# Performance work log

Hardware: AMD Instinct MI355X
Metric: run time of the kernel (lower is better)

Reference implementation:

```python
import jax, jax.numpy as jnp
import numpy as np

B, C, H, W = 8, 96, 160, 320
MH, MW = 4, 4

def setup_inputs() -> dict:
    key = jax.random.key(0)
    k1, k2 = jax.random.split(key)
    feat1 = jax.random.normal(k1, (B, C, H, W), dtype=jnp.float32)
    feat2 = jax.random.normal(k2, (B, C, H, W), dtype=jnp.float32)
    return {"feat1": feat1, "feat2": feat2, "max_offset_h": MH, "max_offset_w": MW}

def reference(feat1, feat2, max_offset_h, max_offset_w):
    # feat1, feat2: [B, C, H, W]
    # cost[b, d, h, w] = sum_c feat1[b,c,h,w] * feat2[b,c,h+dh,w+dw]
    # with (dh, dw) enumerating the (2*mh+1)*(2*mw+1) offset window and
    # zero padding outside image boundaries.
    b, c, h, w = feat1.shape
    mh, mw = max_offset_h, max_offset_w
    padded = jnp.pad(feat2, ((0, 0), (0, 0), (mh, mh), (mw, mw)))
    costs = []
    for dh in range(2 * mh + 1):
        for dw in range(2 * mw + 1):
            shifted = jax.lax.dynamic_slice(padded, (0, 0, dh, dw), (b, c, h, w))
            costs.append(jnp.sum(feat1 * shifted, axis=1))  # [B, H, W]
    return jnp.stack(costs, axis=1)  # [B, (2mh+1)*(2mw+1), H, W]
```

## Files before the change

### kernel.cpp

```cpp
#include <hip/hip_runtime.h>

#define B_   8
#define C_   96
#define H_   160
#define W_   320
#define ND   9
#define NDD  81
#define TH   16
#define TW   16
#define KC   6
#define NCH  16
#define F2ROWS 18
#define F2STRIDE 28
#define F2PLANE (F2ROWS*F2STRIDE)
#define BUFW (KC*F2PLANE)
#define NBUF 3
#define LDSWORDS (NBUF*BUFW)

#define AS1 __attribute__((address_space(1)))
#define AS3 __attribute__((address_space(3)))

__device__ __forceinline__ void gld16(const float* gp, float* lp) {
    __builtin_amdgcn_global_load_lds((const AS1 float*)gp,
                                     (AS3 float*)(unsigned long long)lp, 16, 0, 0);
}

__global__ __launch_bounds__(192, 2)
void corr_kernel(const float* __restrict__ f1g,
                 const float* __restrict__ f2g,
                 float* __restrict__ out)
{
    __shared__ float lds[LDSWORDS];

    const int tid  = threadIdx.x;
    const int wave = tid >> 6;
    const int lane = tid & 63;
    const int row  = lane >> 2;
    const int colb = (lane & 3) << 2;

    const int bid  = blockIdx.x;
    const int ebid = (bid & 7) * 600 + (bid >> 3);
    const int b    = ebid / 600;
    const int t6   = ebid - b * 600;
    const int g    = t6 % 3;
    const int tile = t6 / 3;
    const int by   = tile / 20, bx = tile - by * 20;
    const int x0 = bx * TW, y0 = by * TH;
    const int HWi  = H_ * W_;
    const int r0   = y0 + 3 * g - 4;

    const float* f1b = f1g + (size_t)b * C_ * HWi;
    const float* f2b = f2g + (size_t)b * C_ * HWi;

    const float* f1p = f1b + (y0 + row) * W_ + x0 + colb;

    int so0, so1; bool p0, p1;
    {
        int s, r, c, gy, gx;
        s = lane;      r = s / 7; c = (s - 7 * r) << 2;
        gy = r0 + r;   gx = x0 - 4 + c;
        p0 = (c < 24) & (gy >= 0) & (gy < H_) & (gx >= 0) & (gx <= W_ - 4);
        so0 = gy * W_ + gx;
        s = 64 + lane; r = s / 7; c = (s - 7 * r) << 2;
        gy = r0 + r;   gx = x0 - 4 + c;
        p1 = (s < 126) & (c < 24) & (gy >= 0) & (gy < H_) & (gx >= 0) & (gx <= W_ - 4);
        so1 = gy * W_ + gx;
    }

    const int o0 = (row + wave) * F2STRIDE + colb;

    auto stage = [&](int cb, int bufb) {
#pragma unroll
        for (int j = 0; j < 2; ++j) {
            const int ch = 3 * j + wave;
            const int co = (cb + ch) * HWi;
            float* l = &lds[bufb + ch * F2PLANE];
            if (p0) gld16(f2b + co + so0, l);
            if (p1) gld16(f2b + co + so1, l + 256);
        }
    };

    float4 acc0, acc1, acc2, acc3, acc4, acc5, acc6, acc7, acc8;
    acc0 = acc1 = acc2 = acc3 = acc4 = acc5 = acc6 = acc7 = acc8 = make_float4(0.f, 0.f, 0.f, 0.f);
    float4 P0, P1, P2, P3, P4, P5;

#define F1LOAD(cb) {                                         \
        P0 = *(const float4*)(f1p + (cb) * HWi);             \
        P1 = *(const float4*)(f1p + ((cb) + 1) * HWi);       \
        P2 = *(const float4*)(f1p + ((cb) + 2) * HWi);       \
        P3 = *(const float4*)(f1p + ((cb) + 3) * HWi);       \
        P4 = *(const float4*)(f1p + ((cb) + 4) * HWi);       \
        P5 = *(const float4*)(f1p + ((cb) + 5) * HWi); }

#define STEPD(A, P, e0, e1, e2, e3)                          \
        A.x = fmaf(P.x, e0, A.x);                            \
        A.y = fmaf(P.y, e1, A.y);                            \
        A.z = fmaf(P.z, e2, A.z);                            \
        A.w = fmaf(P.w, e3, A.w);

#define COMPC(c, RB, P) {                                                         \
        const float4 q0 = *(const float4*)&lds[(RB) + c * F2PLANE + o0];          \
        const float4 q1 = *(const float4*)&lds[(RB) + c * F2PLANE + o0 + 4];      \
        const float4 q2 = *(const float4*)&lds[(RB) + c * F2PLANE + o0 + 8];      \
        STEPD(acc0, P, q0.x, q0.y, q0.z, q0.w)                                    \
        STEPD(acc1, P, q0.y, q0.z, q0.w, q1.x)                                    \
        STEPD(acc2, P, q0.z, q0.w, q1.x, q1.y)                                    \
        STEPD(acc3, P, q0.w, q1.x, q1.y, q1.z)                                    \
        STEPD(acc4, P, q1.x, q1.y, q1.z, q1.w)                                    \
        STEPD(acc5, P, q1.y, q1.z, q1.w, q2.x)                                    \
        STEPD(acc6, P, q1.z, q1.w, q2.x, q2.y)                                    \
        STEPD(acc7, P, q1.w, q2.x, q2.y, q2.z)                                    \
        STEPD(acc8, P, q2.x, q2.y, q2.z, q2.w)                                    \
    }
#define CHUNK(RB) COMPC(0,RB,P0) COMPC(1,RB,P1) COMPC(2,RB,P2) \
                  COMPC(3,RB,P3) COMPC(4,RB,P4) COMPC(5,RB,P5)

    for (int t = tid; t < LDSWORDS; t += 192) lds[t] = 0.f;
    __syncthreads();

    stage(0, 0);
    stage(KC, BUFW);

#pragma unroll 1
    for (int k = 0; k < NCH; ++k) {
        if (k < NCH - 1) { asm volatile("s_waitcnt vmcnt(4)" ::: "memory"); }
        else             { asm volatile("s_waitcnt vmcnt(0)" ::: "memory"); }
        __builtin_amdgcn_s_barrier();
        __builtin_amdgcn_sched_barrier(0);
        F1LOAD(KC * k)
        __builtin_amdgcn_sched_barrier(0);
        if (k + 2 < NCH) stage(KC * (k + 2), ((k + 2) % NBUF) * BUFW);
        __builtin_amdgcn_sched_barrier(0);
        const int rb_ = (k % NBUF) * BUFW;
        CHUNK(rb_)
    }

    const int dh = 3 * g + wave;
    const int gy = y0 + row;
    const int gx = x0 + colb;
#define STORED(d) {                                                                 \
        float* op_ = out + (size_t)((b * NDD + dh * ND + d) * H_ + gy) * W_ + gx;   \
        *(float4*)op_ = acc##d; }
    STORED(0) STORED(1) STORED(2) STORED(3) STORED(4)
    STORED(5) STORED(6) STORED(7) STORED(8)
}

extern "C" void kernel_launch(void* const* d_in, const int* in_sizes, int n_in,
                              void* d_out, int out_size, void* d_ws, size_t ws_size,
                              hipStream_t stream)
{
    const float* f1 = (const float*)d_in[0];
    const float* f2 = (const float*)d_in[1];
    float* out = (float*)d_out;
    corr_kernel<<<dim3(4800), 192, 0, stream>>>(f1, f2, out);
}
```

Before: 216.7 us.

## Widen tile to 32 columns with 8 outputs per thread and smaller channel chunks

Doubles the tile width so each thread computes 8 horizontal pixels across 9 horizontal offsets, using 72 accumulators instead of 36. Each set of four LDS float4 reads now feeds twice as many FMAs, and the halo of feat2 is amortized over a wider tile, which cuts redundant global and LDS traffic. The channel chunk size drops to 4 and the staging loop is rewritten so each thread issues one load per channel. The grid is halved. Higher register pressure may hurt occupancy or cause spills under launch_bounds(192,2).

```diff
diff --git a/kernel.cpp b/kernel.cpp
--- a/kernel.cpp
+++ b/kernel.cpp
@@ -7,11 +7,11 @@
 #define ND   9
 #define NDD  81
 #define TH   16
-#define TW   16
-#define KC   6
-#define NCH  16
+#define TW   32
+#define KC   4
+#define NCH  24
 #define F2ROWS 18
-#define F2STRIDE 28
+#define F2STRIDE 40
 #define F2PLANE (F2ROWS*F2STRIDE)
 #define BUFW (KC*F2PLANE)
 #define NBUF 3
@@ -36,15 +36,15 @@
     const int wave = tid >> 6;
     const int lane = tid & 63;
     const int row  = lane >> 2;
-    const int colb = (lane & 3) << 2;
+    const int colb = (lane & 3) << 3;
 
     const int bid  = blockIdx.x;
-    const int ebid = (bid & 7) * 600 + (bid >> 3);
-    const int b    = ebid / 600;
-    const int t6   = ebid - b * 600;
-    const int g    = t6 % 3;
-    const int tile = t6 / 3;
-    const int by   = tile / 20, bx = tile - by * 20;
+    const int ebid = (bid & 7) * 300 + (bid >> 3);
+    const int b    = ebid / 300;
+    const int t3   = ebid - b * 300;
+    const int g    = t3 % 3;
+    const int tile = t3 / 3;
+    const int by   = tile / 10, bx = tile - by * 10;
     const int x0 = bx * TW, y0 = by * TH;
     const int HWi  = H_ * W_;
     const int r0   = y0 + 3 * g - 4;
@@ -54,43 +54,41 @@
 
     const float* f1p = f1b + (y0 + row) * W_ + x0 + colb;
 
-    int so0, so1; bool p0, p1;
+    int soW; bool ppW;
     {
-        int s, r, c, gy, gx;
-        s = lane;      r = s / 7; c = (s - 7 * r) << 2;
-        gy = r0 + r;   gx = x0 - 4 + c;
-        p0 = (c < 24) & (gy >= 0) & (gy < H_) & (gx >= 0) & (gx <= W_ - 4);
-        so0 = gy * W_ + gx;
-        s = 64 + lane; r = s / 7; c = (s - 7 * r) << 2;
-        gy = r0 + r;   gx = x0 - 4 + c;
-        p1 = (s < 126) & (c < 24) & (gy >= 0) & (gy < H_) & (gx >= 0) & (gx <= W_ - 4);
-        so1 = gy * W_ + gx;
+        const int s  = (wave << 6) + lane;
+        const int r  = s / 10, c4 = s - 10 * r;
+        const int gy = r0 + r, gx = x0 - 4 + (c4 << 2);
+        ppW = (s < 180) & (gy >= 0) & (gy < H_) & (gx >= 0) & (gx <= W_ - 4);
+        soW = gy * W_ + gx;
     }
+    const int partoff = wave << 8;
 
     const int o0 = (row + wave) * F2STRIDE + colb;
 
     auto stage = [&](int cb, int bufb) {
 #pragma unroll
-        for (int j = 0; j < 2; ++j) {
-            const int ch = 3 * j + wave;
-            const int co = (cb + ch) * HWi;
-            float* l = &lds[bufb + ch * F2PLANE];
-            if (p0) gld16(f2b + co + so0, l);
-            if (p1) gld16(f2b + co + so1, l + 256);
+        for (int c = 0; c < KC; ++c) {
+            if (ppW) gld16(f2b + (cb + c) * HWi + soW,
+                           &lds[bufb + c * F2PLANE + partoff]);
         }
     };
 
-    float4 acc0, acc1, acc2, acc3, acc4, acc5, acc6, acc7, acc8;
-    acc0 = acc1 = acc2 = acc3 = acc4 = acc5 = acc6 = acc7 = acc8 = make_float4(0.f, 0.f, 0.f, 0.f);
-    float4 P0, P1, P2, P3, P4, P5;
+    float4 accA0, accA1, accA2, accA3, accA4, accA5, accA6, accA7, accA8;
+    float4 accB0, accB1, accB2, accB3, accB4, accB5, accB6, accB7, accB8;
+    accA0=accA1=accA2=accA3=accA4=accA5=accA6=accA7=accA8 = make_float4(0.f,0.f,0.f,0.f);
+    accB0=accB1=accB2=accB3=accB4=accB5=accB6=accB7=accB8 = make_float4(0.f,0.f,0.f,0.f);
+    float4 PA0, PA1, PA2, PA3, PB0, PB1, PB2, PB3;
 
-#define F1LOAD(cb) {                                         \
-        P0 = *(const float4*)(f1p + (cb) * HWi);             \
-        P1 = *(const float4*)(f1p + ((cb) + 1) * HWi);       \
-        P2 = *(const float4*)(f1p + ((cb) + 2) * HWi);       \
-        P3 = *(const float4*)(f1p + ((cb) + 3) * HWi);       \
-        P4 = *(const float4*)(f1p + ((cb) + 4) * HWi);       \
-        P5 = *(const float4*)(f1p + ((cb) + 5) * HWi); }
+#define F1LOAD(cb) {                                              \
+        PA0 = *(const float4*)(f1p + (cb) * HWi);                 \
+        PB0 = *(const float4*)(f1p + (cb) * HWi + 4);             \
+        PA1 = *(const float4*)(f1p + ((cb)+1) * HWi);             \
+        PB1 = *(const float4*)(f1p + ((cb)+1) * HWi + 4);         \
+        PA2 = *(const float4*)(f1p + ((cb)+2) * HWi);             \
+        PB2 = *(const float4*)(f1p + ((cb)+2) * HWi + 4);         \
+        PA3 = *(const float4*)(f1p + ((cb)+3) * HWi);             \
+        PB3 = *(const float4*)(f1p + ((cb)+3) * HWi + 4); }
 
 #define STEPD(A, P, e0, e1, e2, e3)                          \
         A.x = fmaf(P.x, e0, A.x);                            \
@@ -98,22 +96,34 @@
         A.z = fmaf(P.z, e2, A.z);                            \
         A.w = fmaf(P.w, e3, A.w);
 
-#define COMPC(c, RB, P) {                                                         \
+#define COMPC(c, RB, PA, PB) {                                                    \
         const float4 q0 = *(const float4*)&lds[(RB) + c * F2PLANE + o0];          \
         const float4 q1 = *(const float4*)&lds[(RB) + c * F2PLANE + o0 + 4];      \
         const float4 q2 = *(const float4*)&lds[(RB) + c * F2PLANE + o0 + 8];      \
-        STEPD(acc0, P, q0.x, q0.y, q0.z, q0.w)                                    \
-        STEPD(acc1, P, q0.y, q0.z, q0.w, q1.x)                                    \
-        STEPD(acc2, P, q0.z, q0.w, q1.x, q1.y)                                    \
-        STEPD(acc3, P, q0.w, q1.x, q1.y, q1.z)                                    \
-        STEPD(acc4, P, q1.x, q1.y, q1.z, q1.w)                                    \
-        STEPD(acc5, P, q1.y, q1.z, q1.w, q2.x)                                    \
-        STEPD(acc6, P, q1.z, q1.w, q2.x, q2.y)                                    \
-        STEPD(acc7, P, q1.w, q2.x, q2.y, q2.z)                                    \
-        STEPD(acc8, P, q2.x, q2.y, q2.z, q2.w)                                    \
+        const float4 q3 = *(const float4*)&lds[(RB) + c * F2PLANE + o0 + 12];     \
+        const float w[16] = {q0.x,q0.y,q0.z,q0.w,q1.x,q1.y,q1.z,q1.w,            \
+                             q2.x,q2.y,q2.z,q2.w,q3.x,q3.y,q3.z,q3.w};           \
+        STEPD(accA0, PA, w[0], w[1], w[2], w[3])                                  \
+        STEPD(accB0, PB, w[4], w[5], w[6], w[7])                                  \
+        STEPD(accA1, PA, w[1], w[2], w[3], w[4])                                  \
+        STEPD(accB1, PB, w[5], w[6], w[7], w[8])                                  \
+        STEPD(accA2, PA, w[2], w[3], w[4], w[5])                                  \
+        STEPD(accB2, PB, w[6], w[7], w[8], w[9])                                  \
+        STEPD(accA3, PA, w[3], w[4], w[5], w[6])                                  \
+        STEPD(accB3, PB, w[7], w[8], w[9], w[10])                                 \
+        STEPD(accA4, PA, w[4], w[5], w[6], w[7])                                  \
+        STEPD(accB4, PB, w[8], w[9], w[10], w[11])                                \
+        STEPD(accA5, PA, w[5], w[6], w[7], w[8])                                  \
+        STEPD(accB5, PB, w[9], w[10], w[11], w[12])                               \
+        STEPD(accA6, PA, w[6], w[7], w[8], w[9])                                  \
+        STEPD(accB6, PB, w[10], w[11], w[12], w[13])                              \
+        STEPD(accA7, PA, w[7], w[8], w[9], w[10])                                 \
+        STEPD(accB7, PB, w[11], w[12], w[13], w[14])                              \
+        STEPD(accA8, PA, w[8], w[9], w[10], w[11])                                \
+        STEPD(accB8, PB, w[12], w[13], w[14], w[15])                              \
     }
-#define CHUNK(RB) COMPC(0,RB,P0) COMPC(1,RB,P1) COMPC(2,RB,P2) \
-                  COMPC(3,RB,P3) COMPC(4,RB,P4) COMPC(5,RB,P5)
+#define CHUNK(RB) COMPC(0,RB,PA0,PB0) COMPC(1,RB,PA1,PB1) \
+                  COMPC(2,RB,PA2,PB2) COMPC(3,RB,PA3,PB3)
 
     for (int t = tid; t < LDSWORDS; t += 192) lds[t] = 0.f;
     __syncthreads();
@@ -140,7 +150,8 @@
     const int gx = x0 + colb;
 #define STORED(d) {                                                                 \
         float* op_ = out + (size_t)((b * NDD + dh * ND + d) * H_ + gy) * W_ + gx;   \
-        *(float4*)op_ = acc##d; }
+        *(float4*)op_ = accA##d;                                                    \
+        *(float4*)(op_ + 4) = accB##d; }
     STORED(0) STORED(1) STORED(2) STORED(3) STORED(4)
     STORED(5) STORED(6) STORED(7) STORED(8)
 }
@@ -152,5 +163,5 @@
     const float* f1 = (const float*)d_in[0];
     const float* f2 = (const float*)d_in[1];
     float* out = (float*)d_out;
-    corr_kernel<<<dim3(4800), 192, 0, stream>>>(f1, f2, out);
+    corr_kernel<<<dim3(2400), 192, 0, stream>>>(f1, f2, out);
 }
```

New measurement: 197.1 us. 1.1x faster.
